# Kernel optimization log

Measured on AMD Instinct MI355X. Metric: run time of the kernel, lower is better.

Reference implementation:

```python
import jax, jax.numpy as jnp
import numpy as np

N, E, D, L = 50000, 625000, 128, 7
EPS = 1e-7   # GENConv message epsilon
T = 1.0      # softmax aggregation temperature (learn_t=False)
NUM_ATOM_FEATS, ATOM_VOCAB = 9, 64
NUM_BOND_FEATS, BOND_VOCAB = 3, 8


def setup_inputs() -> dict:
    key = jax.random.key(0)
    ks = jax.random.split(key, 9)
    x = jax.random.randint(ks[0], (N, NUM_ATOM_FEATS), 0, ATOM_VOCAB, dtype=jnp.int32)
    edge_index = jax.random.randint(ks[1], (2, E), 0, N, dtype=jnp.int32)
    edge_attr = jax.random.randint(ks[2], (E, NUM_BOND_FEATS), 0, BOND_VOCAB, dtype=jnp.int32)
    atom_emb = jax.random.normal(ks[3], (NUM_ATOM_FEATS, ATOM_VOCAB, D), dtype=jnp.float32) * 0.1
    bond_emb = jax.random.normal(ks[4], (NUM_BOND_FEATS, BOND_VOCAB, D), dtype=jnp.float32) * 0.1
    W = jax.random.normal(ks[5], (L, D, D), dtype=jnp.float32) / np.sqrt(D).astype(np.float32)
    b = jnp.zeros((L, D), dtype=jnp.float32)
    ln_gamma = jnp.ones((L, D), dtype=jnp.float32)
    ln_beta = jnp.zeros((L, D), dtype=jnp.float32)
    return dict(x=x, edge_index=edge_index, edge_attr=edge_attr,
                atom_emb=atom_emb, bond_emb=bond_emb, W=W, b=b,
                ln_gamma=ln_gamma, ln_beta=ln_beta)


def _layer_norm(h, g, bta):
    mu = jnp.mean(h, axis=-1, keepdims=True)
    var = jnp.var(h, axis=-1, keepdims=True)
    return (h - mu) * jax.lax.rsqrt(var + 1e-5) * g + bta


def _gen_conv(h, src, dst, edge_emb, Wl, bl):
    # GENConv: msg = relu(x_j + e) + eps; softmax aggregation over dst; Linear(x + m)
    msg = jax.nn.relu(h[src] + edge_emb) + EPS                 # [E, D]
    logits = msg * T
    seg_max = jax.ops.segment_max(logits, dst, num_segments=N)  # [N, D]
    seg_max = jnp.where(jnp.isfinite(seg_max), seg_max, 0.0)    # empty segments
    e = jnp.exp(logits - seg_max[dst])                          # [E, D]
    denom = jax.ops.segment_sum(e, dst, num_segments=N)         # [N, D]
    alpha = e / (denom[dst] + 1e-16)
    m = jax.ops.segment_sum(alpha * msg, dst, num_segments=N)   # [N, D]
    return (h + m) @ Wl + bl


def reference(x, edge_index, edge_attr, atom_emb, bond_emb, W, b, ln_gamma, ln_beta):
    src, dst = edge_index[0], edge_index[1]
    # AtomEncoder: sum of per-feature embedding lookups -> [N, D]
    h = jnp.sum(atom_emb[jnp.arange(NUM_ATOM_FEATS)[None, :], x], axis=1)
    # BondEncoder (conv_encode_edge=False: encoded once) -> [E, D]
    edge_emb = jnp.sum(bond_emb[jnp.arange(NUM_BOND_FEATS)[None, :], edge_attr], axis=1)
    # res+ block, dropout=0 (no-op)
    h = _gen_conv(h, src, dst, edge_emb, W[0], b[0])
    for layer in range(1, L):
        h2 = jax.nn.relu(_layer_norm(h, ln_gamma[layer - 1], ln_beta[layer - 1]))
        h = _gen_conv(h2, src, dst, edge_emb, W[layer], b[layer]) + h
    h = _layer_norm(h, ln_gamma[L - 1], ln_beta[L - 1])
    return h
```

## Files before the change

kernel.cpp:

```cpp
#include <hip/hip_runtime.h>
#include <hip/hip_fp16.h>
#include <math.h>


constexpr int D = 128;
constexpr int NA = 9;
constexpr int NB = 3;
constexpr float L2E = 1.4426950408889634f;
constexpr float INV_L2E = 0.6931471805599453f;

using half8  = __attribute__((ext_vector_type(8))) _Float16;
using h2v    = __attribute__((ext_vector_type(2))) _Float16;
using floatx4 = __attribute__((ext_vector_type(4))) float;


__global__ void k_hist(const int* __restrict__ dst, int* __restrict__ deg, int E) {
    int e = blockIdx.x * 256 + threadIdx.x;
    if (e < E) atomicAdd(&deg[dst[e]], 1);
}

__global__ void k_scan_a(const int* __restrict__ deg, int* __restrict__ offs,
                         int* __restrict__ bsum, int N) {
    __shared__ int s[256];
    int i = blockIdx.x * 256 + threadIdx.x;
    int v = (i < N) ? deg[i] : 0;
    s[threadIdx.x] = v;
    __syncthreads();
    for (int d = 1; d < 256; d <<= 1) {
        int add = (threadIdx.x >= d) ? s[threadIdx.x - d] : 0;
        __syncthreads();
        s[threadIdx.x] += add;
        __syncthreads();
    }
    if (i < N) offs[i + 1] = s[threadIdx.x];
    if (threadIdx.x == 255) bsum[blockIdx.x] = s[255];
    if (i == 0) offs[0] = 0;
}

__global__ void k_scan_b(const int* __restrict__ bsum, int* __restrict__ bexc, int nb) {
    __shared__ int s[256];
    int t = threadIdx.x;
    int v = (t < nb) ? bsum[t] : 0;
    s[t] = v;
    __syncthreads();
    for (int d = 1; d < 256; d <<= 1) {
        int add = (t >= d) ? s[t - d] : 0;
        __syncthreads();
        s[t] += add;
        __syncthreads();
    }
    if (t < nb) bexc[t] = s[t] - v;
}

__global__ void k_scan_c(int* __restrict__ offs, const int* __restrict__ bexc, int N) {
    int i = blockIdx.x * 256 + threadIdx.x;
    if (i < N) offs[i + 1] += bexc[blockIdx.x];
}

__global__ void k_fill(const int* __restrict__ src, const int* __restrict__ dst,
                       const int* __restrict__ attr, const int* __restrict__ offs,
                       int* __restrict__ cur, int2* __restrict__ recs, int E) {
    int e = blockIdx.x * 256 + threadIdx.x;
    if (e >= E) return;
    int d = dst[e];
    int pos = offs[d] + atomicAdd(&cur[d], 1);
    int cidx = attr[e * 3] * 64 + attr[e * 3 + 1] * 8 + attr[e * 3 + 2];
    recs[pos] = make_int2(src[e], cidx);
}


__global__ void k_dhist(const int* __restrict__ deg, int* __restrict__ dbin, int N) {
    __shared__ int lb[64];
    int t = threadIdx.x;
    if (t < 64) lb[t] = 0;
    __syncthreads();
    int i = blockIdx.x * 256 + t;
    if (i < N) {
        int d = deg[i]; d = d < 63 ? d : 63;
        atomicAdd(&lb[63 - d], 1);
    }
    __syncthreads();
    if (t < 64 && lb[t] > 0) atomicAdd(&dbin[t], lb[t]);
}

__global__ void k_dscan(const int* __restrict__ dbin, int* __restrict__ doff) {
    if (threadIdx.x == 0) {
        int acc = 0;
        for (int b = 0; b < 64; ++b) { doff[b] = acc; acc += dbin[b]; }
    }
}

__global__ void k_dfill(const int* __restrict__ deg, const int* __restrict__ doff,
                        int* __restrict__ dcur, int* __restrict__ perm, int N) {
    __shared__ int lc[64], lbase[64];
    int t = threadIdx.x;
    if (t < 64) lc[t] = 0;
    __syncthreads();
    int i = blockIdx.x * 256 + t;
    int b = 0, rank = 0;
    if (i < N) {
        int d = deg[i]; d = d < 63 ? d : 63;
        b = 63 - d;
        rank = atomicAdd(&lc[b], 1);
    }
    __syncthreads();
    if (t < 64 && lc[t] > 0) lbase[t] = atomicAdd(&dcur[t], lc[t]);
    __syncthreads();
    if (i < N) perm[doff[b] + lbase[b] + rank] = i;
}

__global__ void k_comb(const float* __restrict__ bemb, __half* __restrict__ comb16) {
    int gid = blockIdx.x * 256 + threadIdx.x;
    int c = gid >> 5, q = gid & 31;
    int a0 = c >> 6, a1 = (c >> 3) & 7, a2 = c & 7;
    float4 v0 = *(const float4*)(bemb + (a0)*D + q * 4);
    float4 v1 = *(const float4*)(bemb + (8 + a1) * D + q * 4);
    float4 v2 = *(const float4*)(bemb + (16 + a2) * D + q * 4);
    __half2* c2 = (__half2*)comb16;
    c2[c * 64 + q * 2]     = __floats2half2_rn(L2E * (v0.x + v1.x + v2.x),
                                               L2E * (v0.y + v1.y + v2.y));
    c2[c * 64 + q * 2 + 1] = __floats2half2_rn(L2E * (v0.z + v1.z + v2.z),
                                               L2E * (v0.w + v1.w + v2.w));
}

__global__ void k_wt(const float* __restrict__ W, __half* __restrict__ Wt16, int total) {
    int o = blockIdx.x * 256 + threadIdx.x;
    if (o >= total) return;
    int l = o >> 14;
    int rem = o & 16383;
    int f = rem >> 7, k = rem & 127;
    Wt16[o] = __float2half_rn(W[(l << 14) + k * 128 + f]);
}


__global__ void k_atom(const int* __restrict__ x, const float* __restrict__ aemb,
                       __half* __restrict__ h16, int N) {
    int wid = (blockIdx.x * blockDim.x + threadIdx.x) >> 6;
    int lane = threadIdx.x & 63;
    if (wid >= N) return;
    const int* xr = x + wid * NA;
    float ax = 0.f, ay = 0.f;
#pragma unroll
    for (int f = 0; f < NA; ++f) {
        int v = xr[f];
        const float2 e = *(const float2*)(aemb + (f * 64 + v) * D + 2 * lane);
        ax += e.x; ay += e.y;
    }
    ((__half2*)h16)[wid * 64 + lane] = __floats2half2_rn(ax * L2E, ay * L2E);
}


__global__ __launch_bounds__(256) void k_agg(const __half* __restrict__ h16,
                      const int2* __restrict__ recs,
                      const int* __restrict__ offs, const __half* __restrict__ comb16,
                      const int* __restrict__ perm,
                      __half* __restrict__ t16, int N) {
    int wid = (blockIdx.x * blockDim.x + threadIdx.x) >> 6;
    int lane = threadIdx.x & 63;
    if (wid >= N) return;
    int nid = perm[wid];
    int su = __builtin_amdgcn_readfirstlane(offs[nid]);
    int eu = __builtin_amdgcn_readfirstlane(offs[nid + 1]);
    h2v hm2 = ((const h2v*)h16)[nid * 64 + lane];
    float hsx = (float)hm2[0], hsy = (float)hm2[1];
    if (su >= eu) {
        ((__half2*)t16)[nid * 64 + lane] =
            __floats2half2_rn(hsx * INV_L2E, hsy * INV_L2E);
        return;
    }
    float Sx = 0.f, Sy = 0.f, Wx = 0.f, Wy = 0.f;
    int last = eu - 1;

    const h2v* hrow = (const h2v*)h16 + lane;
    const h2v* crow = (const h2v*)comb16 + lane;

    const h2v zero2 = (h2v)(_Float16)0;
    const h2v eps2  = {(_Float16)(1e-7f * L2E), (_Float16)(1e-7f * L2E)};

    h2v hq[16], cq[16];

    auto load4 = [&](int base, int slot) {
#pragma unroll
        for (int i = 0; i < 4; ++i) {
            int idx = base + i; idx = (idx < last) ? idx : last;
            int2 rr = recs[idx];
            int sj = __builtin_amdgcn_readfirstlane(rr.x);
            int cj = __builtin_amdgcn_readfirstlane(rr.y);
            hq[slot * 4 + i] = hrow[sj * 64];
            cq[slot * 4 + i] = crow[cj * 64];
        }
    };
    auto comp4u = [&](int slot) {
#pragma unroll
        for (int i = 0; i < 4; ++i) {
            h2v m = hq[slot * 4 + i] + cq[slot * 4 + i];
            m = __builtin_elementwise_max(m, zero2);
            m = m + eps2;
            float u0 = (float)m[0], u1 = (float)m[1];
            float px = __builtin_amdgcn_exp2f(u0);
            float py = __builtin_amdgcn_exp2f(u1);
            Sx += px; Sy += py;
            Wx = fmaf(px, u0, Wx);
            Wy = fmaf(py, u1, Wy);
        }
    };
    auto comp4m = [&](int gb, int slot) {
#pragma unroll
        for (int i = 0; i < 4; ++i) {
            h2v m = hq[slot * 4 + i] + cq[slot * 4 + i];
            m = __builtin_elementwise_max(m, zero2);
            m = m + eps2;
            float u0 = (float)m[0], u1 = (float)m[1];
            bool valid = (gb + i) < eu;
            float px = valid ? __builtin_amdgcn_exp2f(u0) : 0.f;
            float py = valid ? __builtin_amdgcn_exp2f(u1) : 0.f;
            Sx += px; Sy += py;
            Wx = fmaf(px, u0, Wx);
            Wy = fmaf(py, u1, Wy);
        }
    };

    load4(su, 0);
    if (su + 4  < eu) load4(su + 4, 1);
    if (su + 8  < eu) load4(su + 8, 2);
    if (su + 12 < eu) load4(su + 12, 3);

    int e = su;
    for (; e + 16 < eu; e += 16) {
        comp4u(0); comp4u(1); comp4u(2); comp4u(3);
        load4(e + 16, 0); load4(e + 20, 1); load4(e + 24, 2); load4(e + 28, 3);
    }
    comp4m(e, 0);
    if (e + 4  < eu) comp4m(e + 4, 1);
    if (e + 8  < eu) comp4m(e + 8, 2);
    if (e + 12 < eu) comp4m(e + 12, 3);

    float tx = (hsx + Wx / (Sx + 1e-16f)) * INV_L2E;
    float ty = (hsy + Wy / (Sy + 1e-16f)) * INV_L2E;
    ((__half2*)t16)[nid * 64 + lane] = __floats2half2_rn(tx, ty);
}


template <int MODE>
__global__ __launch_bounds__(256) void k_gemm(const __half* __restrict__ A16,
                                              const __half* __restrict__ Wt16,
                                              const float* __restrict__ bl,
                                              const __half* __restrict__ res16,
                                              __half* __restrict__ hres16,
                                              const float* __restrict__ g,
                                              const float* __restrict__ bta,
                                              __half* __restrict__ h16,
                                              float* __restrict__ out,
                                              int N, int useRes) {
    int lane = threadIdx.x & 63;
    int wave = threadIdx.x >> 6;
    int quad = lane >> 4, col = lane & 15;
    int node = blockIdx.x * 64 + wave * 16 + col;
    bool nok = node < N;
    int nc = nok ? node : N - 1;

    const __half* arow = A16 + (size_t)nc * 128;
    half8 bfrag[4];
#pragma unroll
    for (int ks = 0; ks < 4; ++ks)
        bfrag[ks] = *(const half8*)(arow + ks * 32 + quad * 8);

    floatx4 acc[8];
#pragma unroll
    for (int ft = 0; ft < 8; ++ft) acc[ft] = (floatx4){0.f, 0.f, 0.f, 0.f};

#pragma unroll
    for (int ft = 0; ft < 8; ++ft) {
        const __half* wrow = Wt16 + (size_t)(ft * 16 + col) * 128;
#pragma unroll
        for (int ks = 0; ks < 4; ++ks) {
            half8 afrag = *(const half8*)(wrow + ks * 32 + quad * 8);
            acc[ft] = __builtin_amdgcn_mfma_f32_16x16x32_f16(afrag, bfrag[ks],
                                                             acc[ft], 0, 0, 0);
        }
    }

    float s = 0.f, ss = 0.f;
#pragma unroll
    for (int ft = 0; ft < 8; ++ft) {
        int f0 = ft * 16 + quad * 4;
        float4 bb = *(const float4*)(bl + f0);
        float o0 = acc[ft][0] + bb.x, o1 = acc[ft][1] + bb.y;
        float o2 = acc[ft][2] + bb.z, o3 = acc[ft][3] + bb.w;
        if (useRes) {
            uint2 rr = *(const uint2*)(res16 + (size_t)nc * 128 + f0);
            __half2 r01 = *(__half2*)&rr.x, r23 = *(__half2*)&rr.y;
            o0 += __low2float(r01); o1 += __high2float(r01);
            o2 += __low2float(r23); o3 += __high2float(r23);
        }
        acc[ft][0] = o0; acc[ft][1] = o1; acc[ft][2] = o2; acc[ft][3] = o3;
        s += (o0 + o1) + (o2 + o3);
        ss += fmaf(o0, o0, o1 * o1) + fmaf(o2, o2, o3 * o3);
        if (MODE == 0 && nok) {
            __half2 h01 = __floats2half2_rn(o0, o1);
            __half2 h23 = __floats2half2_rn(o2, o3);
            uint2 pk = make_uint2(*(unsigned*)&h01, *(unsigned*)&h23);
            *(uint2*)(hres16 + (size_t)node * 128 + f0) = pk;
        }
    }
    s += __shfl_xor(s, 16, 64);  ss += __shfl_xor(ss, 16, 64);
    s += __shfl_xor(s, 32, 64);  ss += __shfl_xor(ss, 32, 64);
    float mu = s * (1.f / 128.f);
    float var = ss * (1.f / 128.f) - mu * mu;
    float rs = rsqrtf(var + 1e-5f);

#pragma unroll
    for (int ft = 0; ft < 8; ++ft) {
        int f0 = ft * 16 + quad * 4;
        float4 gg = *(const float4*)(g + f0);
        float4 bt = *(const float4*)(bta + f0);
        float l0 = (acc[ft][0] - mu) * rs * gg.x + bt.x;
        float l1 = (acc[ft][1] - mu) * rs * gg.y + bt.y;
        float l2 = (acc[ft][2] - mu) * rs * gg.z + bt.z;
        float l3 = (acc[ft][3] - mu) * rs * gg.w + bt.w;
        if (MODE == 0) {
            l0 = fmaxf(l0, 0.f); l1 = fmaxf(l1, 0.f);
            l2 = fmaxf(l2, 0.f); l3 = fmaxf(l3, 0.f);
            if (nok) {
                __half2 h01 = __floats2half2_rn(l0 * L2E, l1 * L2E);
                __half2 h23 = __floats2half2_rn(l2 * L2E, l3 * L2E);
                uint2 pk = make_uint2(*(unsigned*)&h01, *(unsigned*)&h23);
                *(uint2*)(h16 + (size_t)node * 128 + f0) = pk;
            }
        } else {
            if (nok)
                *(float4*)(out + (size_t)node * 128 + f0) =
                    make_float4(l0, l1, l2, l3);
        }
    }
}


extern "C" void kernel_launch(void* const* d_in, const int* in_sizes, int n_in,
                              void* d_out, int out_size, void* d_ws, size_t ws_size,
                              hipStream_t stream) {
    const int*   x    = (const int*)d_in[0];
    const int*   ei   = (const int*)d_in[1];
    const int*   attr = (const int*)d_in[2];
    const float* aemb = (const float*)d_in[3];
    const float* bemb = (const float*)d_in[4];
    const float* Wf   = (const float*)d_in[5];
    const float* bf   = (const float*)d_in[6];
    const float* gam  = (const float*)d_in[7];
    const float* bet  = (const float*)d_in[8];
    float* out = (float*)d_out;

    const int N = in_sizes[0] / NA;
    const int E = in_sizes[1] / 2;
    const int L = in_sizes[5] / (D * D);

    char* ws = (char*)d_ws;
    size_t o = 0;
    auto carve = [&](size_t bytes) -> void* {
        void* p = (void*)(ws + o);
        o += (bytes + 255) & ~(size_t)255;
        return p;
    };
    __half* hres16 = (__half*)carve((size_t)N * D * 2);
    __half* h16    = (__half*)carve((size_t)N * D * 2);
    __half* t16    = (__half*)carve((size_t)N * D * 2);
    int2*   recs   = (int2*)carve((size_t)E * 8);
    __half* comb16 = (__half*)carve(512 * D * 2);
    __half* Wt16   = (__half*)carve((size_t)L * D * D * 2);
    int*    deg    = (int*)carve((size_t)N * 4);
    int*    cur    = (int*)carve((size_t)N * 4);
    int*    offs   = (int*)carve((size_t)(N + 1) * 4);
    int*    perm   = (int*)carve((size_t)N * 4);
    int*    dbin   = (int*)carve(256);
    int*    doff   = (int*)carve(256);
    int*    dcur   = (int*)carve(256);
    int*    bsum   = (int*)carve(4096);
    int*    bexc   = (int*)carve(4096);

    const int* src = ei;
    const int* dst = ei + E;

    hipMemsetAsync(deg, 0, (size_t)N * 4, stream);
    hipMemsetAsync(cur, 0, (size_t)N * 4, stream);
    hipMemsetAsync(dbin, 0, 256, stream);
    hipMemsetAsync(dcur, 0, 256, stream);

    int ebl = (E + 255) / 256;
    int nbl = (N + 255) / 256;
    k_comb<<<64, 256, 0, stream>>>(bemb, comb16);
    int wtot = L * D * D;
    k_wt<<<(wtot + 255) / 256, 256, 0, stream>>>(Wf, Wt16, wtot);
    k_hist<<<ebl, 256, 0, stream>>>(dst, deg, E);
    k_scan_a<<<nbl, 256, 0, stream>>>(deg, offs, bsum, N);
    k_scan_b<<<1, 256, 0, stream>>>(bsum, bexc, nbl);
    k_scan_c<<<nbl, 256, 0, stream>>>(offs, bexc, N);
    k_fill<<<ebl, 256, 0, stream>>>(src, dst, attr, offs, cur, recs, E);
    k_dhist<<<nbl, 256, 0, stream>>>(deg, dbin, N);
    k_dscan<<<1, 64, 0, stream>>>(dbin, doff);
    k_dfill<<<nbl, 256, 0, stream>>>(deg, doff, dcur, perm, N);

    int wbl = (N * 64 + 255) / 256;
    k_atom<<<wbl, 256, 0, stream>>>(x, aemb, h16, N);

    int gbl = (N + 63) / 64;
    for (int l = 0; l < L; ++l) {
        k_agg<<<wbl, 256, 0, stream>>>(h16, recs, offs, comb16, perm, t16, N);
        if (l == L - 1) {
            k_gemm<1><<<gbl, 256, 0, stream>>>(t16, Wt16 + l * D * D, bf + l * D,
                                               hres16, hres16,
                                               gam + l * D, bet + l * D, h16, out,
                                               N, 1);
        } else {
            k_gemm<0><<<gbl, 256, 0, stream>>>(t16, Wt16 + l * D * D, bf + l * D,
                                               hres16, hres16,
                                               gam + l * D, bet + l * D, h16, out,
                                               N, l > 0 ? 1 : 0);
        }
    }
}
```

Baseline: 616.9 us.

## Fuse softmax aggregation into per-layer GEMM kernel via LDS staging

Merges the per-node softmax aggregation and the dense linear/layernorm GEMM into one kernel per layer. Each wave aggregates 16 nodes sequentially and writes the aggregated rows into shared memory, which the MFMA GEMM then reads instead of a global t16 buffer. h is ping-ponged between two buffers, and the degree-sorted node permutation (three kernels) is removed, with the two memsets merged into one. This removes the t16 round trip and several launches, but each wave now handles 16 nodes serially with only 782 blocks, and the loss of degree sorting may hurt load balance and occupancy.

```diff
diff --git a/kernel.cpp b/kernel.cpp
--- a/kernel.cpp
+++ b/kernel.cpp
@@ -68,47 +68,6 @@
     recs[pos] = make_int2(src[e], cidx);
 }
 
-
-__global__ void k_dhist(const int* __restrict__ deg, int* __restrict__ dbin, int N) {
-    __shared__ int lb[64];
-    int t = threadIdx.x;
-    if (t < 64) lb[t] = 0;
-    __syncthreads();
-    int i = blockIdx.x * 256 + t;
-    if (i < N) {
-        int d = deg[i]; d = d < 63 ? d : 63;
-        atomicAdd(&lb[63 - d], 1);
-    }
-    __syncthreads();
-    if (t < 64 && lb[t] > 0) atomicAdd(&dbin[t], lb[t]);
-}
-
-__global__ void k_dscan(const int* __restrict__ dbin, int* __restrict__ doff) {
-    if (threadIdx.x == 0) {
-        int acc = 0;
-        for (int b = 0; b < 64; ++b) { doff[b] = acc; acc += dbin[b]; }
-    }
-}
-
-__global__ void k_dfill(const int* __restrict__ deg, const int* __restrict__ doff,
-                        int* __restrict__ dcur, int* __restrict__ perm, int N) {
-    __shared__ int lc[64], lbase[64];
-    int t = threadIdx.x;
-    if (t < 64) lc[t] = 0;
-    __syncthreads();
-    int i = blockIdx.x * 256 + t;
-    int b = 0, rank = 0;
-    if (i < N) {
-        int d = deg[i]; d = d < 63 ? d : 63;
-        b = 63 - d;
-        rank = atomicAdd(&lc[b], 1);
-    }
-    __syncthreads();
-    if (t < 64 && lc[t] > 0) lbase[t] = atomicAdd(&dcur[t], lc[t]);
-    __syncthreads();
-    if (i < N) perm[doff[b] + lbase[b] + rank] = i;
-}
-
 __global__ void k_comb(const float* __restrict__ bemb, __half* __restrict__ comb16) {
     int gid = blockIdx.x * 256 + threadIdx.x;
     int c = gid >> 5, q = gid & 31;
@@ -150,120 +109,118 @@
 }
 
 
-__global__ __launch_bounds__(256) void k_agg(const __half* __restrict__ h16,
-                      const int2* __restrict__ recs,
-                      const int* __restrict__ offs, const __half* __restrict__ comb16,
-                      const int* __restrict__ perm,
-                      __half* __restrict__ t16, int N) {
-    int wid = (blockIdx.x * blockDim.x + threadIdx.x) >> 6;
-    int lane = threadIdx.x & 63;
-    if (wid >= N) return;
-    int nid = perm[wid];
-    int su = __builtin_amdgcn_readfirstlane(offs[nid]);
-    int eu = __builtin_amdgcn_readfirstlane(offs[nid + 1]);
-    h2v hm2 = ((const h2v*)h16)[nid * 64 + lane];
-    float hsx = (float)hm2[0], hsy = (float)hm2[1];
-    if (su >= eu) {
-        ((__half2*)t16)[nid * 64 + lane] =
-            __floats2half2_rn(hsx * INV_L2E, hsy * INV_L2E);
-        return;
-    }
-    float Sx = 0.f, Sy = 0.f, Wx = 0.f, Wy = 0.f;
-    int last = eu - 1;
-
-    const h2v* hrow = (const h2v*)h16 + lane;
-    const h2v* crow = (const h2v*)comb16 + lane;
-
-    const h2v zero2 = (h2v)(_Float16)0;
-    const h2v eps2  = {(_Float16)(1e-7f * L2E), (_Float16)(1e-7f * L2E)};
-
-    h2v hq[16], cq[16];
-
-    auto load4 = [&](int base, int slot) {
-#pragma unroll
-        for (int i = 0; i < 4; ++i) {
-            int idx = base + i; idx = (idx < last) ? idx : last;
-            int2 rr = recs[idx];
-            int sj = __builtin_amdgcn_readfirstlane(rr.x);
-            int cj = __builtin_amdgcn_readfirstlane(rr.y);
-            hq[slot * 4 + i] = hrow[sj * 64];
-            cq[slot * 4 + i] = crow[cj * 64];
-        }
-    };
-    auto comp4u = [&](int slot) {
-#pragma unroll
-        for (int i = 0; i < 4; ++i) {
-            h2v m = hq[slot * 4 + i] + cq[slot * 4 + i];
-            m = __builtin_elementwise_max(m, zero2);
-            m = m + eps2;
-            float u0 = (float)m[0], u1 = (float)m[1];
-            float px = __builtin_amdgcn_exp2f(u0);
-            float py = __builtin_amdgcn_exp2f(u1);
-            Sx += px; Sy += py;
-            Wx = fmaf(px, u0, Wx);
-            Wy = fmaf(py, u1, Wy);
-        }
-    };
-    auto comp4m = [&](int gb, int slot) {
-#pragma unroll
-        for (int i = 0; i < 4; ++i) {
-            h2v m = hq[slot * 4 + i] + cq[slot * 4 + i];
-            m = __builtin_elementwise_max(m, zero2);
-            m = m + eps2;
-            float u0 = (float)m[0], u1 = (float)m[1];
-            bool valid = (gb + i) < eu;
-            float px = valid ? __builtin_amdgcn_exp2f(u0) : 0.f;
-            float py = valid ? __builtin_amdgcn_exp2f(u1) : 0.f;
-            Sx += px; Sy += py;
-            Wx = fmaf(px, u0, Wx);
-            Wy = fmaf(py, u1, Wy);
-        }
-    };
-
-    load4(su, 0);
-    if (su + 4  < eu) load4(su + 4, 1);
-    if (su + 8  < eu) load4(su + 8, 2);
-    if (su + 12 < eu) load4(su + 12, 3);
-
-    int e = su;
-    for (; e + 16 < eu; e += 16) {
-        comp4u(0); comp4u(1); comp4u(2); comp4u(3);
-        load4(e + 16, 0); load4(e + 20, 1); load4(e + 24, 2); load4(e + 28, 3);
-    }
-    comp4m(e, 0);
-    if (e + 4  < eu) comp4m(e + 4, 1);
-    if (e + 8  < eu) comp4m(e + 8, 2);
-    if (e + 12 < eu) comp4m(e + 12, 3);
-
-    float tx = (hsx + Wx / (Sx + 1e-16f)) * INV_L2E;
-    float ty = (hsy + Wy / (Sy + 1e-16f)) * INV_L2E;
-    ((__half2*)t16)[nid * 64 + lane] = __floats2half2_rn(tx, ty);
-}
-
-
 template <int MODE>
-__global__ __launch_bounds__(256) void k_gemm(const __half* __restrict__ A16,
-                                              const __half* __restrict__ Wt16,
-                                              const float* __restrict__ bl,
-                                              const __half* __restrict__ res16,
-                                              __half* __restrict__ hres16,
-                                              const float* __restrict__ g,
-                                              const float* __restrict__ bta,
-                                              __half* __restrict__ h16,
-                                              float* __restrict__ out,
-                                              int N, int useRes) {
+__global__ __launch_bounds__(256) void k_layer(const __half* __restrict__ h16in,
+                                               const int2* __restrict__ recs,
+                                               const int* __restrict__ offs,
+                                               const __half* __restrict__ comb16,
+                                               const __half* __restrict__ Wt16,
+                                               const float* __restrict__ bl,
+                                               const __half* __restrict__ res16,
+                                               __half* __restrict__ hres16,
+                                               const float* __restrict__ g,
+                                               const float* __restrict__ bta,
+                                               __half* __restrict__ h16out,
+                                               float* __restrict__ out,
+                                               int N, int useRes) {
+    __shared__ alignas(16) _Float16 tlds[64 * 136];
+
     int lane = threadIdx.x & 63;
     int wave = threadIdx.x >> 6;
     int quad = lane >> 4, col = lane & 15;
-    int node = blockIdx.x * 64 + wave * 16 + col;
+    int m0 = blockIdx.x * 64;
+    int base = m0 + wave * 16;
+
+    const h2v* hrow = (const h2v*)h16in + lane;
+    const h2v* crow = (const h2v*)comb16 + lane;
+    const h2v zero2 = (h2v)(_Float16)0;
+    const h2v eps2  = {(_Float16)(1e-7f * L2E), (_Float16)(1e-7f * L2E)};
+
+    for (int j = 0; j < 16; ++j) {
+        int nid = base + j;
+        float tx = 0.f, ty = 0.f;
+        if (nid < N) {
+            int su = __builtin_amdgcn_readfirstlane(offs[nid]);
+            int eu = __builtin_amdgcn_readfirstlane(offs[nid + 1]);
+            h2v hm2 = hrow[nid * 64];
+            float hsx = (float)hm2[0], hsy = (float)hm2[1];
+            if (su >= eu) {
+                tx = hsx * INV_L2E; ty = hsy * INV_L2E;
+            } else {
+                float Sx = 0.f, Sy = 0.f, Wx = 0.f, Wy = 0.f;
+                int last = eu - 1;
+                h2v hq[16], cq[16];
+                auto load4 = [&](int b4, int slot) {
+#pragma unroll
+                    for (int i = 0; i < 4; ++i) {
+                        int idx = b4 + i; idx = (idx < last) ? idx : last;
+                        int2 rr = recs[idx];
+                        int sj = __builtin_amdgcn_readfirstlane(rr.x);
+                        int cj = __builtin_amdgcn_readfirstlane(rr.y);
+                        hq[slot * 4 + i] = hrow[sj * 64];
+                        cq[slot * 4 + i] = crow[cj * 64];
+                    }
+                };
+                auto comp4u = [&](int slot) {
+#pragma unroll
+                    for (int i = 0; i < 4; ++i) {
+                        h2v m = hq[slot * 4 + i] + cq[slot * 4 + i];
+                        m = __builtin_elementwise_max(m, zero2);
+                        m = m + eps2;
+                        float u0 = (float)m[0], u1 = (float)m[1];
+                        float px = __builtin_amdgcn_exp2f(u0);
+                        float py = __builtin_amdgcn_exp2f(u1);
+                        Sx += px; Sy += py;
+                        Wx = fmaf(px, u0, Wx);
+                        Wy = fmaf(py, u1, Wy);
+                    }
+                };
+                auto comp4m = [&](int gb, int slot) {
+#pragma unroll
+                    for (int i = 0; i < 4; ++i) {
+                        h2v m = hq[slot * 4 + i] + cq[slot * 4 + i];
+                        m = __builtin_elementwise_max(m, zero2);
+                        m = m + eps2;
+                        float u0 = (float)m[0], u1 = (float)m[1];
+                        bool valid = (gb + i) < eu;
+                        float px = valid ? __builtin_amdgcn_exp2f(u0) : 0.f;
+                        float py = valid ? __builtin_amdgcn_exp2f(u1) : 0.f;
+                        Sx += px; Sy += py;
+                        Wx = fmaf(px, u0, Wx);
+                        Wy = fmaf(py, u1, Wy);
+                    }
+                };
+                load4(su, 0);
+                if (su + 4  < eu) load4(su + 4, 1);
+                if (su + 8  < eu) load4(su + 8, 2);
+                if (su + 12 < eu) load4(su + 12, 3);
+                int e = su;
+                for (; e + 16 < eu; e += 16) {
+                    comp4u(0); comp4u(1); comp4u(2); comp4u(3);
+                    load4(e + 16, 0); load4(e + 20, 1);
+                    load4(e + 24, 2); load4(e + 28, 3);
+                }
+                comp4m(e, 0);
+                if (e + 4  < eu) comp4m(e + 4, 1);
+                if (e + 8  < eu) comp4m(e + 8, 2);
+                if (e + 12 < eu) comp4m(e + 12, 3);
+                tx = (hsx + Wx / (Sx + 1e-16f)) * INV_L2E;
+                ty = (hsy + Wy / (Sy + 1e-16f)) * INV_L2E;
+            }
+        }
+        h2v tv = {(_Float16)tx, (_Float16)ty};
+        *(h2v*)(tlds + (wave * 16 + j) * 136 + lane * 2) = tv;
+    }
+
+    int node = base + col;
     bool nok = node < N;
     int nc = nok ? node : N - 1;
 
-    const __half* arow = A16 + (size_t)nc * 128;
+    const _Float16* trow = tlds + (wave * 16 + col) * 136;
     half8 bfrag[4];
 #pragma unroll
     for (int ks = 0; ks < 4; ++ks)
-        bfrag[ks] = *(const half8*)(arow + ks * 32 + quad * 8);
+        bfrag[ks] = *(const half8*)(trow + ks * 32 + quad * 8);
 
     floatx4 acc[8];
 #pragma unroll
@@ -325,7 +282,7 @@
                 __half2 h01 = __floats2half2_rn(l0 * L2E, l1 * L2E);
                 __half2 h23 = __floats2half2_rn(l2 * L2E, l3 * L2E);
                 uint2 pk = make_uint2(*(unsigned*)&h01, *(unsigned*)&h23);
-                *(uint2*)(h16 + (size_t)node * 128 + f0) = pk;
+                *(uint2*)(h16out + (size_t)node * 128 + f0) = pk;
             }
         } else {
             if (nok)
@@ -362,28 +319,22 @@
         return p;
     };
     __half* hres16 = (__half*)carve((size_t)N * D * 2);
-    __half* h16    = (__half*)carve((size_t)N * D * 2);
-    __half* t16    = (__half*)carve((size_t)N * D * 2);
+    __half* hA16   = (__half*)carve((size_t)N * D * 2);
+    __half* hB16   = (__half*)carve((size_t)N * D * 2);
     int2*   recs   = (int2*)carve((size_t)E * 8);
     __half* comb16 = (__half*)carve(512 * D * 2);
     __half* Wt16   = (__half*)carve((size_t)L * D * D * 2);
     int*    deg    = (int*)carve((size_t)N * 4);
     int*    cur    = (int*)carve((size_t)N * 4);
     int*    offs   = (int*)carve((size_t)(N + 1) * 4);
-    int*    perm   = (int*)carve((size_t)N * 4);
-    int*    dbin   = (int*)carve(256);
-    int*    doff   = (int*)carve(256);
-    int*    dcur   = (int*)carve(256);
     int*    bsum   = (int*)carve(4096);
     int*    bexc   = (int*)carve(4096);
 
     const int* src = ei;
     const int* dst = ei + E;
 
-    hipMemsetAsync(deg, 0, (size_t)N * 4, stream);
-    hipMemsetAsync(cur, 0, (size_t)N * 4, stream);
-    hipMemsetAsync(dbin, 0, 256, stream);
-    hipMemsetAsync(dcur, 0, 256, stream);
+    size_t degRound = ((size_t)N * 4 + 255) & ~(size_t)255;
+    hipMemsetAsync(deg, 0, degRound * 2, stream);
 
     int ebl = (E + 255) / 256;
     int nbl = (N + 255) / 256;
@@ -395,26 +346,26 @@
     k_scan_b<<<1, 256, 0, stream>>>(bsum, bexc, nbl);
     k_scan_c<<<nbl, 256, 0, stream>>>(offs, bexc, N);
     k_fill<<<ebl, 256, 0, stream>>>(src, dst, attr, offs, cur, recs, E);
-    k_dhist<<<nbl, 256, 0, stream>>>(deg, dbin, N);
-    k_dscan<<<1, 64, 0, stream>>>(dbin, doff);
-    k_dfill<<<nbl, 256, 0, stream>>>(deg, doff, dcur, perm, N);
 
     int wbl = (N * 64 + 255) / 256;
-    k_atom<<<wbl, 256, 0, stream>>>(x, aemb, h16, N);
+    k_atom<<<wbl, 256, 0, stream>>>(x, aemb, hA16, N);
 
     int gbl = (N + 63) / 64;
     for (int l = 0; l < L; ++l) {
-        k_agg<<<wbl, 256, 0, stream>>>(h16, recs, offs, comb16, perm, t16, N);
+        const __half* hin  = (l & 1) ? hB16 : hA16;
+        __half*       hout = (l & 1) ? hA16 : hB16;
         if (l == L - 1) {
-            k_gemm<1><<<gbl, 256, 0, stream>>>(t16, Wt16 + l * D * D, bf + l * D,
-                                               hres16, hres16,
-                                               gam + l * D, bet + l * D, h16, out,
-                                               N, 1);
+            k_layer<1><<<gbl, 256, 0, stream>>>(hin, recs, offs, comb16,
+                                                Wt16 + l * D * D, bf + l * D,
+                                                hres16, hres16,
+                                                gam + l * D, bet + l * D,
+                                                hout, out, N, 1);
         } else {
-            k_gemm<0><<<gbl, 256, 0, stream>>>(t16, Wt16 + l * D * D, bf + l * D,
-                                               hres16, hres16,
-                                               gam + l * D, bet + l * D, h16, out,
-                                               N, l > 0 ? 1 : 0);
-        }
-    }
-}
+            k_layer<0><<<gbl, 256, 0, stream>>>(hin, recs, offs, comb16,
+                                                Wt16 + l * D * D, bf + l * D,
+                                                hres16, hres16,
+                                                gam + l * D, bet + l * D,
+                                                hout, out, N, l > 0 ? 1 : 0);
+        }
+    }
+}
```

After: 832.3 us. +34.9%, slower.
